# Kernel optimization log

Hardware: AMD Instinct MI355X
Metric: run time of the kernel (lower is better)

Reference implementation:

```python
import jax, jax.numpy as jnp
import numpy as np

IN_CH = 512
HID = 512
SCALE = 1.0 / np.sqrt(16.0)  # hard-coded 16**0.5 in source, not sqrt(hidden)


def setup_inputs() -> dict:
    key = jax.random.key(0)
    ks = jax.random.split(key, 9)
    B, T = 8, 2048
    lim = 1.0 / np.sqrt(IN_CH)
    return {
        "q": jax.random.normal(ks[0], (B, T, IN_CH), dtype=jnp.float32),
        "k": jax.random.normal(ks[1], (B, T, IN_CH), dtype=jnp.float32),
        "v": jax.random.normal(ks[2], (B, T, IN_CH), dtype=jnp.float32),
        "Wq": jax.random.uniform(ks[3], (IN_CH, HID), jnp.float32, -lim, lim),
        "bq": jax.random.uniform(ks[4], (HID,), jnp.float32, -lim, lim),
        "Wk": jax.random.uniform(ks[5], (IN_CH, HID), jnp.float32, -lim, lim),
        "bk": jax.random.uniform(ks[6], (HID,), jnp.float32, -lim, lim),
        "Wv": jax.random.uniform(ks[7], (IN_CH, HID), jnp.float32, -lim, lim),
        "bv": jax.random.uniform(ks[8], (HID,), jnp.float32, -lim, lim),
    }


def reference(q, k, v, Wq, bq, Wk, bk, Wv, bv):
    # Linear projections: [B,T,F] @ [F,H] + [H]
    query = jnp.einsum("btf,fh->bth", q, Wq) + bq
    key_p = jnp.einsum("btf,fh->bth", k, Wk) + bk
    value = jnp.einsum("btf,fh->bth", v, Wv) + bv
    # energy: [B,T,T], scaled by fixed 1/sqrt(16)
    energy = jnp.einsum("bth,bsh->bts", query, key_p) * SCALE
    attn = jax.nn.softmax(energy, axis=-1)
    # weighted sum: [B,T,H]
    return jnp.einsum("bts,bsh->bth", attn, value)
```

## Files before the change

kernel.cpp:

```cpp
#include <hip/hip_runtime.h>
#include <stdint.h>

typedef __bf16 bf16;
typedef bf16 bf16x8 __attribute__((ext_vector_type(8)));
typedef float f32x4 __attribute__((ext_vector_type(4)));

#define MFMA(a, b, c) __builtin_amdgcn_mfma_f32_16x16x32_bf16(a, b, c, 0, 0, 0)

#define SCALE_L2E 0.3606737602222409f
#define M0 16.0f

__device__ __forceinline__ void gload_lds16(const void* g, void* l) {
  __builtin_amdgcn_global_load_lds(
      (const __attribute__((address_space(1))) uint32_t*)g,
      (__attribute__((address_space(3))) uint32_t*)l, 16, 0, 0);
}

__global__ void k_wtrans(const float* __restrict__ Wq, const float* __restrict__ Wk,
                         const float* __restrict__ Wv, bf16* __restrict__ Wt) {
  int idx = blockIdx.x * 256 + threadIdx.x;
  int z = idx >> 18;
  int r = idx & 262143;
  int n = r >> 9, k = r & 511;
  const float* W = (z == 0) ? Wq : (z == 1) ? Wk : Wv;
  Wt[idx] = (bf16)W[k * 512 + n];
}

__global__ __launch_bounds__(256, 2) void k_proj(
    const float* __restrict__ q, const float* __restrict__ k, const float* __restrict__ v,
    const bf16* __restrict__ Wt, const float* __restrict__ bq, const float* __restrict__ bk,
    const float* __restrict__ bv, bf16* __restrict__ Qp, bf16* __restrict__ Kp,
    bf16* __restrict__ Vp) {
  int z = blockIdx.z;
  const float* A = (z == 0) ? q : (z == 1) ? k : v;
  const float* bias = (z == 0) ? bq : (z == 1) ? bk : bv;
  bf16* C = (z == 0) ? Qp : (z == 1) ? Kp : Vp;
  const bf16* Bw = Wt + (size_t)z * 512 * 512;
  float sc = (z == 0) ? SCALE_L2E : 1.0f;

  int m0 = blockIdx.x * 128, n0 = blockIdx.y * 128;
  __shared__ bf16 As[128 * 40];
  __shared__ bf16 Bs[128 * 40];

  int tid = threadIdx.x;
  int wave = tid >> 6, lane = tid & 63, qr = lane & 15, quad = lane >> 4;
  int wm = (wave >> 1) * 64, wn = (wave & 1) * 64;

  f32x4 acc[4][4];
  for (int mi = 0; mi < 4; mi++)
    for (int ni = 0; ni < 4; ni++) acc[mi][ni] = (f32x4){0.f, 0.f, 0.f, 0.f};

  for (int k0 = 0; k0 < 512; k0 += 32) {
    __syncthreads();
    for (int i = 0; i < 2; i++) {
      int ch = i * 256 + tid;
      int row = ch >> 2, c = ch & 3;
      const float4* src = (const float4*)(A + (size_t)(m0 + row) * 512 + k0 + c * 8);
      float4 x = src[0], y = src[1];
      bf16x8 t;
      t[0] = (bf16)x.x; t[1] = (bf16)x.y; t[2] = (bf16)x.z; t[3] = (bf16)x.w;
      t[4] = (bf16)y.x; t[5] = (bf16)y.y; t[6] = (bf16)y.z; t[7] = (bf16)y.w;
      *(bf16x8*)&As[row * 40 + c * 8] = t;
      *(bf16x8*)&Bs[row * 40 + c * 8] =
          *(const bf16x8*)(Bw + (size_t)(n0 + row) * 512 + k0 + c * 8);
    }
    __syncthreads();
    bf16x8 af[4], bfv[4];
    for (int mi = 0; mi < 4; mi++)
      af[mi] = *(bf16x8*)&As[(wm + mi * 16 + qr) * 40 + quad * 8];
    for (int ni = 0; ni < 4; ni++)
      bfv[ni] = *(bf16x8*)&Bs[(wn + ni * 16 + qr) * 40 + quad * 8];
    for (int mi = 0; mi < 4; mi++)
      for (int ni = 0; ni < 4; ni++) acc[mi][ni] = MFMA(af[mi], bfv[ni], acc[mi][ni]);
  }

  for (int ni = 0; ni < 4; ni++) {
    int col = n0 + wn + ni * 16 + qr;
    float bz = bias[col];
    for (int mi = 0; mi < 4; mi++) {
      int rbase = m0 + wm + mi * 16 + quad * 4;
      for (int r = 0; r < 4; r++)
        C[(size_t)(rbase + r) * 512 + col] = (bf16)((acc[mi][ni][r] + bz) * sc);
    }
  }
}

__global__ void k_vtrans(const bf16* __restrict__ Vp, bf16* __restrict__ Vtp) {
  __shared__ bf16 tile[32][33];
  int x = threadIdx.x, y = threadIdx.y;
  int t0 = blockIdx.x * 32, h0 = blockIdx.y * 32, b = blockIdx.z;
  for (int kk = 0; kk < 4; kk++)
    tile[y + 8 * kk][x] = Vp[(size_t)(b * 2048 + t0 + y + 8 * kk) * 512 + h0 + x];
  __syncthreads();
  for (int kk = 0; kk < 4; kk++)
    Vtp[(size_t)(b * 512 + h0 + y + 8 * kk) * 2048 + t0 + x] = tile[x][y + 8 * kk];
}

__global__ __launch_bounds__(256, 2) void k_qk(const bf16* __restrict__ Qp,
                                               const bf16* __restrict__ Kp,
                                               bf16* __restrict__ P,
                                               float* __restrict__ Lpart) {
  __shared__ bf16 As[128 * 32];
  __shared__ bf16 Bs[128 * 32];
  int b = blockIdx.z;
  const bf16* A = Qp + (size_t)b * 2048 * 512;
  const bf16* B = Kp + (size_t)b * 2048 * 512;
  bf16* Pb = P + (size_t)b * 2048 * 2048;
  int m0 = blockIdx.x * 128, n0 = blockIdx.y * 128;
  int tid = threadIdx.x;
  int wave = tid >> 6, lane = tid & 63, qr = lane & 15, quad = lane >> 4;
  int wm = (wave >> 1) * 64, wn = (wave & 1) * 64;

  f32x4 acc[4][4];
  for (int mi = 0; mi < 4; mi++)
    for (int ni = 0; ni < 4; ni++) acc[mi][ni] = (f32x4){0.f, 0.f, 0.f, 0.f};

  for (int k0 = 0; k0 < 512; k0 += 32) {
    __syncthreads();
    for (int i = 0; i < 2; i++) {
      int ch = i * 256 + tid;
      int row = ch >> 2, c = ch & 3;
      gload_lds16(A + (size_t)(m0 + row) * 512 + k0 + c * 8, &As[ch * 8]);
      gload_lds16(B + (size_t)(n0 + row) * 512 + k0 + c * 8, &Bs[ch * 8]);
    }
    __syncthreads();
    bf16x8 af[4], bfv[4];
    for (int mi = 0; mi < 4; mi++)
      af[mi] = *(bf16x8*)&As[(wm + mi * 16 + qr) * 32 + quad * 8];
    for (int ni = 0; ni < 4; ni++)
      bfv[ni] = *(bf16x8*)&Bs[(wn + ni * 16 + qr) * 32 + quad * 8];
    for (int mi = 0; mi < 4; mi++)
      for (int ni = 0; ni < 4; ni++) acc[mi][ni] = MFMA(af[mi], bfv[ni], acc[mi][ni]);
  }

  int slice = blockIdx.y * 2 + (wave & 1);
  float* Lp = Lpart + (size_t)slice * 16384 + b * 2048;
  for (int mi = 0; mi < 4; mi++) {
    int rowb = m0 + wm + mi * 16 + quad * 4;
    for (int r = 0; r < 4; r++) {
      float s = 0.f;
      bf16* prow = Pb + (size_t)(rowb + r) * 2048 + n0 + wn + qr;
      for (int ni = 0; ni < 4; ni++) {
        float e = exp2f(acc[mi][ni][r] - M0);
        prow[ni * 16] = (bf16)e;
        s += e;
      }
      s += __shfl_xor(s, 1);
      s += __shfl_xor(s, 2);
      s += __shfl_xor(s, 4);
      s += __shfl_xor(s, 8);
      if (qr == 0) Lp[rowb + r] = s;
    }
  }
}

__global__ void k_lred(const float* __restrict__ Lpart, float* __restrict__ Linv) {
  int i = blockIdx.x * 256 + threadIdx.x;
  float s = 0.f;
  for (int j = 0; j < 32; j++) s += Lpart[(size_t)j * 16384 + i];
  Linv[i] = 1.0f / s;
}

__global__ __launch_bounds__(256, 2) void k_pv(const bf16* __restrict__ P,
                                               const bf16* __restrict__ Vtp,
                                               const float* __restrict__ Linv,
                                               float* __restrict__ out) {
  __shared__ bf16 As[128 * 32];
  __shared__ bf16 Bs[128 * 32];
  int b = blockIdx.z;
  const bf16* A = P + (size_t)b * 2048 * 2048;
  const bf16* B = Vtp + (size_t)b * 512 * 2048;
  int m0 = blockIdx.x * 128, n0 = blockIdx.y * 128;
  int tid = threadIdx.x;
  int wave = tid >> 6, lane = tid & 63, qr = lane & 15, quad = lane >> 4;
  int wm = (wave >> 1) * 64, wn = (wave & 1) * 64;

  f32x4 acc[4][4];
  for (int mi = 0; mi < 4; mi++)
    for (int ni = 0; ni < 4; ni++) acc[mi][ni] = (f32x4){0.f, 0.f, 0.f, 0.f};

  for (int k0 = 0; k0 < 2048; k0 += 32) {
    __syncthreads();
    for (int i = 0; i < 2; i++) {
      int ch = i * 256 + tid;
      int row = ch >> 2, c = ch & 3;
      gload_lds16(A + (size_t)(m0 + row) * 2048 + k0 + c * 8, &As[ch * 8]);
      gload_lds16(B + (size_t)(n0 + row) * 2048 + k0 + c * 8, &Bs[ch * 8]);
    }
    __syncthreads();
    bf16x8 af[4], bfv[4];
    for (int mi = 0; mi < 4; mi++)
      af[mi] = *(bf16x8*)&As[(wm + mi * 16 + qr) * 32 + quad * 8];
    for (int ni = 0; ni < 4; ni++)
      bfv[ni] = *(bf16x8*)&Bs[(wn + ni * 16 + qr) * 32 + quad * 8];
    for (int mi = 0; mi < 4; mi++)
      for (int ni = 0; ni < 4; ni++) acc[mi][ni] = MFMA(af[mi], bfv[ni], acc[mi][ni]);
  }

  for (int mi = 0; mi < 4; mi++) {
    int rowb = m0 + wm + mi * 16 + quad * 4;
    float linv[4];
    for (int r = 0; r < 4; r++) linv[r] = Linv[b * 2048 + rowb + r];
    for (int ni = 0; ni < 4; ni++) {
      int col = n0 + wn + ni * 16 + qr;
      float* og = out + (size_t)(b * 2048 + rowb) * 512 + col;
      for (int r = 0; r < 4; r++) og[(size_t)r * 512] = acc[mi][ni][r] * linv[r];
    }
  }
}

extern "C" void kernel_launch(void* const* d_in, const int* in_sizes, int n_in,
                              void* d_out, int out_size, void* d_ws, size_t ws_size,
                              hipStream_t stream) {
  (void)in_sizes; (void)n_in; (void)out_size; (void)ws_size;
  const float* q  = (const float*)d_in[0];
  const float* k  = (const float*)d_in[1];
  const float* v  = (const float*)d_in[2];
  const float* Wq = (const float*)d_in[3];
  const float* bq = (const float*)d_in[4];
  const float* Wk = (const float*)d_in[5];
  const float* bk = (const float*)d_in[6];
  const float* Wv = (const float*)d_in[7];
  const float* bv = (const float*)d_in[8];
  float* out = (float*)d_out;

  char* ws = (char*)d_ws;
  bf16* Wt    = (bf16*)(ws);
  bf16* Qp    = (bf16*)(ws + 1572864);
  bf16* Kp    = (bf16*)(ws + 18350080);
  bf16* Vp    = (bf16*)(ws + 35127296);
  bf16* Vtp   = (bf16*)(ws + 51904512);
  bf16* P     = (bf16*)(ws + 68681728);
  float* Lpart = (float*)(ws + 135790592);
  float* Linv  = (float*)(ws + 137887744);

  k_wtrans<<<3072, 256, 0, stream>>>(Wq, Wk, Wv, Wt);
  k_proj<<<dim3(128, 4, 3), 256, 0, stream>>>(q, k, v, Wt, bq, bk, bv, Qp, Kp, Vp);
  k_vtrans<<<dim3(64, 16, 8), dim3(32, 8, 1), 0, stream>>>(Vp, Vtp);
  k_qk<<<dim3(16, 16, 8), 256, 0, stream>>>(Qp, Kp, P, Lpart);
  k_lred<<<64, 256, 0, stream>>>(Lpart, Linv);
  k_pv<<<dim3(16, 4, 8), 256, 0, stream>>>(P, Vtp, Linv, out);
}
```

Before: 299.7 us.

## Fuse V transpose into projection epilogue and retile PV for occupancy

The projection kernel now writes the V projection directly in transposed [B,H,T] layout, which removes the separate k_vtrans kernel and its intermediate buffer round trip. The weight tile is loaded with direct global-to-LDS loads. The PV GEMM is retiled to 64-row M tiles, which doubles the grid to 1024 blocks and raises the occupancy hints on several kernels. The transposed V stores are 8-byte scattered writes with a 2048-element stride, which may coalesce poorly, and the smaller PV tiles reduce reuse of the B tile.

```diff
diff --git a/kernel.cpp b/kernel.cpp
--- a/kernel.cpp
+++ b/kernel.cpp
@@ -26,21 +26,19 @@
   Wt[idx] = (bf16)W[k * 512 + n];
 }
 
-__global__ __launch_bounds__(256, 2) void k_proj(
+__global__ __launch_bounds__(256, 4) void k_proj(
     const float* __restrict__ q, const float* __restrict__ k, const float* __restrict__ v,
     const bf16* __restrict__ Wt, const float* __restrict__ bq, const float* __restrict__ bk,
     const float* __restrict__ bv, bf16* __restrict__ Qp, bf16* __restrict__ Kp,
-    bf16* __restrict__ Vp) {
+    bf16* __restrict__ Vtp) {
   int z = blockIdx.z;
   const float* A = (z == 0) ? q : (z == 1) ? k : v;
   const float* bias = (z == 0) ? bq : (z == 1) ? bk : bv;
-  bf16* C = (z == 0) ? Qp : (z == 1) ? Kp : Vp;
   const bf16* Bw = Wt + (size_t)z * 512 * 512;
-  float sc = (z == 0) ? SCALE_L2E : 1.0f;
 
   int m0 = blockIdx.x * 128, n0 = blockIdx.y * 128;
   __shared__ bf16 As[128 * 40];
-  __shared__ bf16 Bs[128 * 40];
+  __shared__ bf16 Bs[128 * 32];
 
   int tid = threadIdx.x;
   int wave = tid >> 6, lane = tid & 63, qr = lane & 15, quad = lane >> 4;
@@ -55,48 +53,52 @@
     for (int i = 0; i < 2; i++) {
       int ch = i * 256 + tid;
       int row = ch >> 2, c = ch & 3;
+      gload_lds16(Bw + (size_t)(n0 + row) * 512 + k0 + c * 8, &Bs[ch * 8]);
       const float4* src = (const float4*)(A + (size_t)(m0 + row) * 512 + k0 + c * 8);
       float4 x = src[0], y = src[1];
       bf16x8 t;
       t[0] = (bf16)x.x; t[1] = (bf16)x.y; t[2] = (bf16)x.z; t[3] = (bf16)x.w;
       t[4] = (bf16)y.x; t[5] = (bf16)y.y; t[6] = (bf16)y.z; t[7] = (bf16)y.w;
       *(bf16x8*)&As[row * 40 + c * 8] = t;
-      *(bf16x8*)&Bs[row * 40 + c * 8] =
-          *(const bf16x8*)(Bw + (size_t)(n0 + row) * 512 + k0 + c * 8);
     }
     __syncthreads();
     bf16x8 af[4], bfv[4];
     for (int mi = 0; mi < 4; mi++)
       af[mi] = *(bf16x8*)&As[(wm + mi * 16 + qr) * 40 + quad * 8];
     for (int ni = 0; ni < 4; ni++)
-      bfv[ni] = *(bf16x8*)&Bs[(wn + ni * 16 + qr) * 40 + quad * 8];
+      bfv[ni] = *(bf16x8*)&Bs[(wn + ni * 16 + qr) * 32 + quad * 8];
     for (int mi = 0; mi < 4; mi++)
       for (int ni = 0; ni < 4; ni++) acc[mi][ni] = MFMA(af[mi], bfv[ni], acc[mi][ni]);
   }
 
-  for (int ni = 0; ni < 4; ni++) {
-    int col = n0 + wn + ni * 16 + qr;
-    float bz = bias[col];
-    for (int mi = 0; mi < 4; mi++) {
-      int rbase = m0 + wm + mi * 16 + quad * 4;
-      for (int r = 0; r < 4; r++)
-        C[(size_t)(rbase + r) * 512 + col] = (bf16)((acc[mi][ni][r] + bz) * sc);
-    }
-  }
-}
-
-__global__ void k_vtrans(const bf16* __restrict__ Vp, bf16* __restrict__ Vtp) {
-  __shared__ bf16 tile[32][33];
-  int x = threadIdx.x, y = threadIdx.y;
-  int t0 = blockIdx.x * 32, h0 = blockIdx.y * 32, b = blockIdx.z;
-  for (int kk = 0; kk < 4; kk++)
-    tile[y + 8 * kk][x] = Vp[(size_t)(b * 2048 + t0 + y + 8 * kk) * 512 + h0 + x];
-  __syncthreads();
-  for (int kk = 0; kk < 4; kk++)
-    Vtp[(size_t)(b * 512 + h0 + y + 8 * kk) * 2048 + t0 + x] = tile[x][y + 8 * kk];
-}
-
-__global__ __launch_bounds__(256, 2) void k_qk(const bf16* __restrict__ Qp,
+  if (z == 2) {
+    for (int ni = 0; ni < 4; ni++) {
+      int col = n0 + wn + ni * 16 + qr;
+      float bz = bias[col];
+      for (int mi = 0; mi < 4; mi++) {
+        int rbase = m0 + wm + mi * 16 + quad * 4;
+        int bb = rbase >> 11, tt = rbase & 2047;
+        bf16 tmp[4];
+        for (int r = 0; r < 4; r++) tmp[r] = (bf16)(acc[mi][ni][r] + bz);
+        *(uint64_t*)(Vtp + ((size_t)(bb * 512 + col)) * 2048 + tt) = *(uint64_t*)tmp;
+      }
+    }
+  } else {
+    bf16* C = (z == 0) ? Qp : Kp;
+    float sc = (z == 0) ? SCALE_L2E : 1.0f;
+    for (int ni = 0; ni < 4; ni++) {
+      int col = n0 + wn + ni * 16 + qr;
+      float bz = bias[col];
+      for (int mi = 0; mi < 4; mi++) {
+        int rbase = m0 + wm + mi * 16 + quad * 4;
+        for (int r = 0; r < 4; r++)
+          C[(size_t)(rbase + r) * 512 + col] = (bf16)((acc[mi][ni][r] + bz) * sc);
+      }
+    }
+  }
+}
+
+__global__ __launch_bounds__(256, 3) void k_qk(const bf16* __restrict__ Qp,
                                                const bf16* __restrict__ Kp,
                                                bf16* __restrict__ P,
                                                float* __restrict__ Lpart) {
@@ -161,43 +163,46 @@
   Linv[i] = 1.0f / s;
 }
 
-__global__ __launch_bounds__(256, 2) void k_pv(const bf16* __restrict__ P,
+__global__ __launch_bounds__(256, 4) void k_pv(const bf16* __restrict__ P,
                                                const bf16* __restrict__ Vtp,
                                                const float* __restrict__ Linv,
                                                float* __restrict__ out) {
-  __shared__ bf16 As[128 * 32];
+  __shared__ bf16 As[64 * 32];
   __shared__ bf16 Bs[128 * 32];
   int b = blockIdx.z;
   const bf16* A = P + (size_t)b * 2048 * 2048;
   const bf16* B = Vtp + (size_t)b * 512 * 2048;
-  int m0 = blockIdx.x * 128, n0 = blockIdx.y * 128;
+  int m0 = blockIdx.x * 64, n0 = blockIdx.y * 128;
   int tid = threadIdx.x;
   int wave = tid >> 6, lane = tid & 63, qr = lane & 15, quad = lane >> 4;
-  int wm = (wave >> 1) * 64, wn = (wave & 1) * 64;
-
-  f32x4 acc[4][4];
-  for (int mi = 0; mi < 4; mi++)
+  int wm = (wave >> 1) * 32, wn = (wave & 1) * 64;
+
+  f32x4 acc[2][4];
+  for (int mi = 0; mi < 2; mi++)
     for (int ni = 0; ni < 4; ni++) acc[mi][ni] = (f32x4){0.f, 0.f, 0.f, 0.f};
 
   for (int k0 = 0; k0 < 2048; k0 += 32) {
     __syncthreads();
+    {
+      int row = tid >> 2, c = tid & 3;
+      gload_lds16(A + (size_t)(m0 + row) * 2048 + k0 + c * 8, &As[tid * 8]);
+    }
     for (int i = 0; i < 2; i++) {
       int ch = i * 256 + tid;
       int row = ch >> 2, c = ch & 3;
-      gload_lds16(A + (size_t)(m0 + row) * 2048 + k0 + c * 8, &As[ch * 8]);
       gload_lds16(B + (size_t)(n0 + row) * 2048 + k0 + c * 8, &Bs[ch * 8]);
     }
     __syncthreads();
-    bf16x8 af[4], bfv[4];
-    for (int mi = 0; mi < 4; mi++)
+    bf16x8 af[2], bfv[4];
+    for (int mi = 0; mi < 2; mi++)
       af[mi] = *(bf16x8*)&As[(wm + mi * 16 + qr) * 32 + quad * 8];
     for (int ni = 0; ni < 4; ni++)
       bfv[ni] = *(bf16x8*)&Bs[(wn + ni * 16 + qr) * 32 + quad * 8];
-    for (int mi = 0; mi < 4; mi++)
+    for (int mi = 0; mi < 2; mi++)
       for (int ni = 0; ni < 4; ni++) acc[mi][ni] = MFMA(af[mi], bfv[ni], acc[mi][ni]);
   }
 
-  for (int mi = 0; mi < 4; mi++) {
+  for (int mi = 0; mi < 2; mi++) {
     int rowb = m0 + wm + mi * 16 + quad * 4;
     float linv[4];
     for (int r = 0; r < 4; r++) linv[r] = Linv[b * 2048 + rowb + r];
@@ -225,19 +230,17 @@
   float* out = (float*)d_out;
 
   char* ws = (char*)d_ws;
-  bf16* Wt    = (bf16*)(ws);
-  bf16* Qp    = (bf16*)(ws + 1572864);
-  bf16* Kp    = (bf16*)(ws + 18350080);
-  bf16* Vp    = (bf16*)(ws + 35127296);
-  bf16* Vtp   = (bf16*)(ws + 51904512);
-  bf16* P     = (bf16*)(ws + 68681728);
-  float* Lpart = (float*)(ws + 135790592);
-  float* Linv  = (float*)(ws + 137887744);
+  bf16* Wt     = (bf16*)(ws);
+  bf16* Qp     = (bf16*)(ws + 1572864);
+  bf16* Kp     = (bf16*)(ws + 18350080);
+  bf16* Vtp    = (bf16*)(ws + 35127296);
+  bf16* P      = (bf16*)(ws + 51904512);
+  float* Lpart = (float*)(ws + 119013376);
+  float* Linv  = (float*)(ws + 121110528);
 
   k_wtrans<<<3072, 256, 0, stream>>>(Wq, Wk, Wv, Wt);
-  k_proj<<<dim3(128, 4, 3), 256, 0, stream>>>(q, k, v, Wt, bq, bk, bv, Qp, Kp, Vp);
-  k_vtrans<<<dim3(64, 16, 8), dim3(32, 8, 1), 0, stream>>>(Vp, Vtp);
+  k_proj<<<dim3(128, 4, 3), 256, 0, stream>>>(q, k, v, Wt, bq, bk, bv, Qp, Kp, Vtp);
   k_qk<<<dim3(16, 16, 8), 256, 0, stream>>>(Qp, Kp, P, Lpart);
   k_lred<<<64, 256, 0, stream>>>(Lpart, Linv);
-  k_pv<<<dim3(16, 4, 8), 256, 0, stream>>>(P, Vtp, Linv, out);
-}
+  k_pv<<<dim3(32, 4, 8), 256, 0, stream>>>(P, Vtp, Linv, out);
+}
```

Measured after the change: 304.7 us. No clear change (+1.7%).
